# Kernel tuning notes

Hardware: AMD Instinct MI355X
Metric: run time of the kernel (lower is better)

## Reference

```python
import jax, jax.numpy as jnp
import numpy as np
from jax import lax

DN = ('NCHW', 'OIHW', 'NCHW')
EPS = 1e-12  # torch F.normalize eps


def _conv(x, w, b, groups=1):
    y = lax.conv_general_dilated(x, w, window_strides=(1, 1), padding='SAME',
                                 dimension_numbers=DN, feature_group_count=groups)
    return y + b[None, :, None, None]


def _l2norm(x):
    # normalize along last axis, matching torch.nn.functional.normalize
    n = jnp.sqrt(jnp.sum(x * x, axis=-1, keepdims=True))
    return x / jnp.maximum(n, EPS)


def setup_inputs() -> dict:
    key = jax.random.key(0)
    ks = jax.random.split(key, 5)
    dim, heads = 192, 8
    b, h, w = 4, 256, 256
    return {
        'x': jax.random.normal(ks[0], (b, dim, h, w), jnp.float32),
        'qkv_w': jax.random.normal(ks[1], (3 * dim, dim, 1, 1), jnp.float32) * 0.05,
        'qkv_b': jnp.zeros((3 * dim,), jnp.float32),
        'dw_w': jax.random.normal(ks[2], (3 * dim, 1, 3, 3), jnp.float32) * 0.05,
        'dw_b': jnp.zeros((3 * dim,), jnp.float32),
        'scale': jnp.ones((1, heads, 1, 1), jnp.float32),
        'proj_w': jax.random.normal(ks[3], (dim, dim, 1, 1), jnp.float32) * 0.05,
        'proj_b': jnp.zeros((dim,), jnp.float32),
    }


def reference(x, qkv_w, qkv_b, dw_w, dw_b, scale, proj_w, proj_b):
    b, c, h, w = x.shape
    heads = scale.shape[1]
    hc = c // heads  # per-head channels
    hw = h * w

    qkv = _conv(x, qkv_w, qkv_b)                       # [b, 3c, h, w]
    qkv = _conv(qkv, dw_w, dw_b, groups=3 * c)          # depthwise 3x3
    q, k, v = jnp.split(qkv, 3, axis=1)                 # each [b, c, h, w]

    # b (head c) h w -> b head c (h w)
    def heads_flat(t):
        return t.reshape(b, heads, hc, hw)

    q = _l2norm(heads_flat(q))
    k = _l2norm(heads_flat(k))
    v = heads_flat(v)

    attn = jnp.einsum('bncs,bnds->bncd', q, k) * scale   # [b, heads, hc, hc]
    attn = jax.nn.softmax(attn, axis=-1)
    out = jnp.einsum('bncd,bnds->bncs', attn, v)         # [b, heads, hc, hw]
    out = out.reshape(b, c, h, w)
    return _conv(out, proj_w, proj_b)
```

## Files before the change

### kernel.cpp

```cpp
#include <hip/hip_runtime.h>
#include <hip/hip_bf16.h>

typedef unsigned short u16;
typedef __attribute__((ext_vector_type(8))) short bf16x8;
typedef __attribute__((ext_vector_type(4))) float f32x4;

#define MFMA16(a,b,c) __builtin_amdgcn_mfma_f32_16x16x32_bf16(a,b,c,0,0,0)

__device__ __forceinline__ u16 f2bf(float f) {
  union { float f; unsigned u; } v; v.f = f;
  return (u16)((v.u + 0x7fffu + ((v.u >> 16) & 1u)) >> 16);
}
__device__ __forceinline__ float bf2f(u16 h) {
  union { unsigned u; float f; } v; v.u = ((unsigned)h) << 16;
  return v.f;
}
__device__ __forceinline__ int qkv_ch(int g, int c) {
  if (g < 8) return (c < 24) ? (g*24 + c) : (192 + g*24 + (c - 24));
  return 384 + (g - 8)*48 + c;
}

__global__ __launch_bounds__(256) void k0_wb(
    const float* __restrict__ qkv_w, const float* __restrict__ qkv_b,
    u16* __restrict__ Wb, float* __restrict__ Bp) {
  int j = blockIdx.x*256 + threadIdx.x;
  int m = j / 192, k = j % 192;
  Wb[j] = f2bf(qkv_w[qkv_ch(m/48, m%48)*192 + k]);
  if (j < 576) Bp[j] = qkv_b[qkv_ch(j/48, j%48)];
}

__global__ __launch_bounds__(512) void k1_qkv(
    const float* __restrict__ x, const u16* __restrict__ Wb,
    const float* __restrict__ Bp, u16* __restrict__ qkv1) {
  int blk = blockIdx.x;
  int bb = blk >> 9, nb = blk & 511;
  int s0 = nb << 7;
  int t = threadIdx.x;
  int lane = t & 63, wid = t >> 6;
  int lg = lane >> 4, lr = lane & 15;
  int wr = wid >> 1, wc = wid & 1;

  __shared__ __align__(16) u16 Bt[24*128*8];

  const float* xb = x + (size_t)bb*(192*65536) + s0;
  {
    int px4 = t & 31, kO = t >> 5;
    #pragma unroll
    for (int rnd = 0; rnd < 2; ++rnd, kO += 16) {
      if (kO < 24) {
        float4 f[8];
        #pragma unroll
        for (int j = 0; j < 8; ++j)
          f[j] = *(const float4*)(xb + (size_t)(kO*8 + j)*65536 + px4*4);
        #pragma unroll
        for (int e = 0; e < 4; ++e) {
          int px = px4*4 + e;
          bf16x8 hh;
          #pragma unroll
          for (int j = 0; j < 8; ++j)
            hh[j] = (short)f2bf(((const float*)&f[j])[e]);
          int byte = (kO*2048 + px*16) ^ ((px4 & 7) << 4);
          *(bf16x8*)((char*)Bt + byte) = hh;
        }
      }
    }
  }
  __syncthreads();

  #pragma unroll 1
  for (int pass = 0; pass < 3; ++pass) {
    int g = pass*4 + wr;
    bf16x8 af[3][6];
    #pragma unroll
    for (int mt = 0; mt < 3; ++mt) {
      const u16* wrp = Wb + (size_t)(g*48 + mt*16 + lr)*192 + lg*8;
      #pragma unroll
      for (int ks = 0; ks < 6; ++ks)
        af[mt][ks] = *(const bf16x8*)(wrp + ks*32);
    }
    f32x4 acc[3][4];
    #pragma unroll
    for (int mt = 0; mt < 3; ++mt)
      #pragma unroll
      for (int nt = 0; nt < 4; ++nt)
        acc[mt][nt] = (f32x4){0.f, 0.f, 0.f, 0.f};

    #pragma unroll
    for (int ks = 0; ks < 6; ++ks) {
      bf16x8 bf[4];
      #pragma unroll
      for (int nt = 0; nt < 4; ++nt) {
        int px = wc*64 + nt*16 + lr;
        int byte = ((ks*4 + lg)*2048 + px*16) ^ (((px >> 2) & 7) << 4);
        bf[nt] = *(const bf16x8*)((const char*)Bt + byte);
      }
      #pragma unroll
      for (int mt = 0; mt < 3; ++mt)
        #pragma unroll
        for (int nt = 0; nt < 4; ++nt)
          acc[mt][nt] = MFMA16(af[mt][ks], bf[nt], acc[mt][nt]);
    }

    u16* dst = qkv1 + ((size_t)(bb*12 + g)*65536 + s0)*48;
    #pragma unroll
    for (int mt = 0; mt < 3; ++mt) {
      float4 bv = *(const float4*)(Bp + g*48 + mt*16 + lg*4);
      #pragma unroll
      for (int nt = 0; nt < 4; ++nt) {
        int px = wc*64 + nt*16 + lr;
        ushort4 o;
        o.x = f2bf(acc[mt][nt][0] + bv.x);
        o.y = f2bf(acc[mt][nt][1] + bv.y);
        o.z = f2bf(acc[mt][nt][2] + bv.z);
        o.w = f2bf(acc[mt][nt][3] + bv.w);
        *(ushort4*)(dst + (size_t)px*48 + mt*16 + lg*4) = o;
      }
    }
  }
}

__global__ __launch_bounds__(256) void k2_dw(
    const u16* __restrict__ qkv1, const float* __restrict__ dw_w,
    const float* __restrict__ dw_b, u16* __restrict__ vd,
    float* __restrict__ partials) {
  int tile = blockIdx.x;
  int tx = tile & 15, ty = tile >> 4;
  int g  = blockIdx.y;
  int bb = blockIdx.z;
  int x0 = tx << 4, y0 = ty << 4;
  int t = threadIdx.x;

  __shared__ __align__(16) u16 buf0[9472];
  __shared__ __align__(16) u16 buf1[14784];
  __shared__ float w9[432];
  __shared__ float wb[48];
  float* stg = (float*)buf0;

  for (int j = t; j < 480; j += 256) {
    if (j < 432) { int c = j / 9; w9[j] = dw_w[qkv_ch(g, c)*9 + (j % 9)]; }
    else         { int c = j - 432; wb[c] = dw_b[qkv_ch(g, c)]; }
  }
  if (g < 8)
    for (int j = t; j < 2112; j += 256) buf1[12672 + j] = 0;

  const u16* src = qkv1 + (size_t)(bb*12 + g) * (65536*48);

  #pragma unroll 1
  for (int h = 0; h < 3; ++h) {
    if (h) __syncthreads();
    #pragma unroll
    for (int r = 0; r < 3; ++r) {
      int j = t + (r << 8);
      if (j < 648) {
        int hp = j >> 1, c16 = j & 1;
        int hr = hp / 18, hc = hp - hr*18;
        int hy = y0 - 1 + hr, hx = x0 - 1 + hc;
        uint4 v = {0u, 0u, 0u, 0u};
        if (hy >= 0 && hy < 256 && hx >= 0 && hx < 256)
          v = *(const uint4*)(src + ((size_t)hy*256 + hx)*48 + h*16 + c16*8);
        const u16* us = (const u16*)&v;
        int base = c16*(8*456 + 8) + hr*24 + hc;
        #pragma unroll
        for (int cc = 0; cc < 8; ++cc)
          buf0[base + cc*456] = us[cc];
      }
    }
    __syncthreads();

    {
      int lc = t & 15, row = t >> 4;
      int c = h*16 + lc;
      float wv[9];
      #pragma unroll
      for (int i = 0; i < 9; ++i) wv[i] = w9[c*9 + i];
      float bias = wb[c];
      int ibase = lc*456 + ((lc >> 3) << 3);
      float rowf[3][18];
      #pragma unroll
      for (int dy = 0; dy < 3; ++dy) {
        int base = ibase + (row + dy)*24;
        u16 hrow[18];
        *(uint4*)(hrow)      = *(const uint4*)(buf0 + base);
        *(uint4*)(hrow + 8)  = *(const uint4*)(buf0 + base + 8);
        *(uint*)(hrow + 16)  = *(const uint*)(buf0 + base + 16);
        #pragma unroll
        for (int i2 = 0; i2 < 18; ++i2) rowf[dy][i2] = bf2f(hrow[i2]);
      }
      float o[16];
      #pragma unroll
      for (int p = 0; p < 16; ++p) {
        float a = bias;
        #pragma unroll
        for (int dy = 0; dy < 3; ++dy)
          a += rowf[dy][p]*wv[dy*3] + rowf[dy][p+1]*wv[dy*3+1] + rowf[dy][p+2]*wv[dy*3+2];
        o[p] = a;
      }
      if (g < 8) {
        unsigned ow[8];
        #pragma unroll
        for (int i = 0; i < 8; ++i)
          asm volatile("v_cvt_pk_bf16_f32 %0, %1, %2"
                       : "=v"(ow[i]) : "v"(o[2*i]), "v"(o[2*i + 1]));
        u16* dsth = buf1 + c*264 + row*16;
        *(uint4*)(dsth)     = make_uint4(ow[0], ow[1], ow[2], ow[3]);
        *(uint4*)(dsth + 8) = make_uint4(ow[4], ow[5], ow[6], ow[7]);
      } else {
        int obase = row*792 + c;
        #pragma unroll
        for (int p = 0; p < 16; ++p)
          buf1[obase + p*48] = f2bf(o[p]);
      }
    }
  }
  __syncthreads();

  if (g < 8) {
    int lane = t & 63, w = t >> 6;
    int lr = lane & 15, lg = lane >> 4;
    f32x4 cc4[8];
    #pragma unroll
    for (int i = 0; i < 8; ++i) cc4[i] = (f32x4){0.f, 0.f, 0.f, 0.f};
    #pragma unroll
    for (int ks = 0; ks < 2; ++ks) {
      int pxb = w*64 + ks*32 + lg*8;
      bf16x8 aq[2], ak[2];
      aq[0] = *(const bf16x8*)(buf1 + (size_t)lr*264 + pxb);
      aq[1] = *(const bf16x8*)(buf1 + (size_t)(16 + lr)*264 + pxb);
      ak[0] = *(const bf16x8*)(buf1 + (size_t)(24 + lr)*264 + pxb);
      ak[1] = *(const bf16x8*)(buf1 + (size_t)(40 + lr)*264 + pxb);
      cc4[0] = MFMA16(aq[0], ak[0], cc4[0]);
      cc4[1] = MFMA16(aq[0], ak[1], cc4[1]);
      cc4[2] = MFMA16(aq[1], ak[0], cc4[2]);
      cc4[3] = MFMA16(aq[1], ak[1], cc4[3]);
      cc4[4] = MFMA16(aq[0], aq[0], cc4[4]);
      cc4[5] = MFMA16(aq[1], aq[1], cc4[5]);
      cc4[6] = MFMA16(ak[0], ak[0], cc4[6]);
      cc4[7] = MFMA16(ak[1], ak[1], cc4[7]);
    }
    #pragma unroll
    for (int tile2 = 0; tile2 < 4; ++tile2) {
      float* sp = stg + w*1088 + tile2*272 + lr;
      #pragma unroll
      for (int r = 0; r < 4; ++r)
        sp[(lg*4 + r)*17] = cc4[tile2][r];
    }
    {
      int r = lr - lg*4;
      if (r >= 0 && r < 4) {
        stg[4352 + w*96 + lr]      = cc4[4][r];
        stg[4352 + w*96 + 48 + lr] = cc4[6][r];
        if (lr < 8) {
          stg[4352 + w*96 + 16 + lr]      = cc4[5][r];
          stg[4352 + w*96 + 48 + 16 + lr] = cc4[7][r];
        }
      }
    }
    __syncthreads();
    float* pdst = partials + (((size_t)bb*256 + tile)*8 + g) * 640;
    for (int e = t; e < 624; e += 256) {
      float s = 0.f;
      if (e < 576) {
        int c = e / 24, d = e % 24;
        int off = ((c >> 4)*2 + (d >> 4))*272 + (c & 15)*17 + (d & 15);
        #pragma unroll
        for (int w2 = 0; w2 < 4; ++w2) s += stg[w2*1088 + off];
      } else {
        int cc2 = e - 576;
        int qk = cc2 / 24, ch = cc2 % 24;
        #pragma unroll
        for (int w2 = 0; w2 < 4; ++w2) s += stg[4352 + w2*96 + qk*48 + ch];
      }
      pdst[e] = s;
    }
  } else {
    u16* dst = vd + (size_t)bb * (65536*192);
    #pragma unroll
    for (int i = 0; i < 6; ++i) {
      int j = t + (i << 8);
      int pp = j / 6, c16 = j % 6;
      int py = pp >> 4, px = pp & 15;
      size_t s = (size_t)(y0 + py)*256 + (x0 + px);
      uint4 v = *(const uint4*)(buf1 + pp*48 + py*24 + c16*8);
      *(uint4*)(dst + s*192 + (g - 8)*48 + c16*8) = v;
    }
  }
}

__global__ __launch_bounds__(256) void k3a(
    const float* __restrict__ partials, float* __restrict__ G2) {
  int bb = blockIdx.x, h = blockIdx.y, ch = blockIdx.z;
  int t = threadIdx.x;
  for (int e = t; e < 624; e += 256) {
    const float* p = partials + ((size_t)(bb*256 + ch*32)*8 + h)*640 + e;
    float s = 0.f;
    #pragma unroll 4
    for (int blk = 0; blk < 32; ++blk) s += p[(size_t)blk * (8*640)];
    G2[(size_t)((bb*8 + h)*8 + ch)*640 + e] = s;
  }
}

__global__ __launch_bounds__(256) void k3b(
    const float* __restrict__ G2, const float* __restrict__ scale,
    const float* __restrict__ proj_w, u16* __restrict__ M) {
  int bb = blockIdx.x, h = blockIdx.y;
  int t = threadIdx.x;
  __shared__ float Gh[640];
  __shared__ float attn[24*24];
  for (int j = t; j < 640; j += 256) {
    float s = 0.f;
    #pragma unroll
    for (int ch = 0; ch < 8; ++ch)
      s += G2[(size_t)((bb*8 + h)*8 + ch)*640 + j];
    Gh[j] = s;
  }
  __syncthreads();
  if (t < 24) {
    int c = t;
    float qn = fmaxf(sqrtf(fmaxf(Gh[576 + c], 0.f)), 1e-12f);
    float sc = scale[h];
    float L[24];
    float mx = -1e30f;
    #pragma unroll
    for (int d = 0; d < 24; ++d) {
      float kn = fmaxf(sqrtf(fmaxf(Gh[600 + d], 0.f)), 1e-12f);
      L[d] = Gh[c*24 + d] / (qn * kn) * sc;
      mx = fmaxf(mx, L[d]);
    }
    float ssum = 0.f;
    #pragma unroll
    for (int d = 0; d < 24; ++d) { L[d] = __expf(L[d] - mx); ssum += L[d]; }
    float inv = 1.f / ssum;
    #pragma unroll
    for (int d = 0; d < 24; ++d) attn[c*24 + d] = L[d] * inv;
  }
  __syncthreads();
  for (int j = t; j < 4608; j += 256) {
    int co = j / 24, d = j % 24;
    const float* Pr = proj_w + co*192 + h*24;
    float s = 0.f;
    #pragma unroll
    for (int c = 0; c < 24; ++c) s += Pr[c] * attn[c*24 + d];
    M[(size_t)bb*36864 + co*192 + h*24 + d] = f2bf(s);
  }
}

__global__ __launch_bounds__(256) void k4_out(
    const u16* __restrict__ vd, const u16* __restrict__ M,
    const float* __restrict__ proj_b, float* __restrict__ out) {
  int p = blockIdx.x;
  int xcd = p & 7, q = p >> 3;
  int pr = xcd*512 + q;
  int bb = pr >> 10, nb = pr & 1023;
  int s0 = nb << 6;
  int t = threadIdx.x;
  int lane = t & 63, wid = t >> 6;
  int lg = lane >> 4, lr = lane & 15;

  const u16* Mb = M + (size_t)bb*36864;
  const u16* Bs = vd + ((size_t)bb*65536 + s0)*192;

  f32x4 acc[3][4];
  #pragma unroll
  for (int mt = 0; mt < 3; ++mt)
    #pragma unroll
    for (int nt = 0; nt < 4; ++nt)
      acc[mt][nt] = (f32x4){0.f, 0.f, 0.f, 0.f};

  #pragma unroll
  for (int ks = 0; ks < 6; ++ks) {
    bf16x8 bf[4], af[3];
    #pragma unroll
    for (int nt = 0; nt < 4; ++nt)
      bf[nt] = *(const bf16x8*)(Bs + (size_t)(nt*16 + lr)*192 + ks*32 + lg*8);
    #pragma unroll
    for (int mt = 0; mt < 3; ++mt)
      af[mt] = *(const bf16x8*)(Mb + (size_t)(wid*48 + mt*16 + lr)*192 + ks*32 + lg*8);
    #pragma unroll
    for (int mt = 0; mt < 3; ++mt)
      #pragma unroll
      for (int nt = 0; nt < 4; ++nt)
        acc[mt][nt] = MFMA16(af[mt], bf[nt], acc[mt][nt]);
  }

  float* dst = out + (size_t)bb*(192*65536) + s0;
  #pragma unroll
  for (int mt = 0; mt < 3; ++mt) {
    int m0 = wid*48 + mt*16 + lg*4;
    #pragma unroll
    for (int r = 0; r < 4; ++r) {
      float bias = proj_b[m0 + r];
      #pragma unroll
      for (int nt = 0; nt < 4; ++nt)
        dst[(size_t)(m0 + r)*65536 + nt*16 + lr] = acc[mt][nt][r] + bias;
    }
  }
}

extern "C" void kernel_launch(void* const* d_in, const int* in_sizes, int n_in,
                              void* d_out, int out_size, void* d_ws, size_t ws_size,
                              hipStream_t stream) {
  (void)in_sizes; (void)n_in; (void)out_size; (void)ws_size;
  const float* x      = (const float*)d_in[0];
  const float* qkv_w  = (const float*)d_in[1];
  const float* qkv_b  = (const float*)d_in[2];
  const float* dw_w   = (const float*)d_in[3];
  const float* dw_b   = (const float*)d_in[4];
  const float* scale  = (const float*)d_in[5];
  const float* proj_w = (const float*)d_in[6];
  const float* proj_b = (const float*)d_in[7];
  float* out = (float*)d_out;
  char* ws = (char*)d_ws;

  u16*   qkv1     = (u16*)(ws);
  u16*   vd       = (u16*)(ws + 301989888ULL);
  float* partials = (float*)(ws + 402653184ULL);
  u16*   Wb       = (u16*)(ws + 402653184ULL);
  float* Bp       = (float*)(ws + 402653184ULL + 221184ULL);
  float* G2       = (float*)(ws);
  u16*   M        = (u16*)(ws + 1048576ULL);

  k0_wb<<<dim3(432), dim3(256), 0, stream>>>(qkv_w, qkv_b, Wb, Bp);
  k1_qkv<<<dim3(2048), dim3(512), 0, stream>>>(x, Wb, Bp, qkv1);
  k2_dw<<<dim3(256, 12, 4), dim3(256), 0, stream>>>(qkv1, dw_w, dw_b, vd, partials);
  k3a<<<dim3(4, 8, 8), dim3(256), 0, stream>>>(partials, G2);
  k3b<<<dim3(4, 8), dim3(256), 0, stream>>>(G2, scale, proj_w, M);
  k4_out<<<dim3(4096), dim3(256), 0, stream>>>(vd, M, proj_b, out);
}
```

Baseline: 525.0 us.

## Shrink QKV GEMM tiles to 64 pixels, stream weights per k-step, use packed bf16 convert

The QKV 1x1-conv GEMM kernel now processes 64 pixels per block with 256 threads instead of 128 pixels with 512 threads, halving shared memory per block and requesting 5 blocks per CU. Weight fragments are now loaded per k-step instead of being held for all six k-steps, which lowers register pressure and should raise occupancy. Float-to-bf16 conversion now uses the hardware v_cvt_pk_bf16_f32 instruction in place of manual integer rounding. The trade-off is more global weight reads, since each block reloads the weights for twice as many tiles, and possible differences in rounding behaviour from the hardware convert.

New measurement: 566.7 us. +8.0%, slower.

```diff
diff --git a/kernel.cpp b/kernel.cpp
--- a/kernel.cpp
+++ b/kernel.cpp
@@ -29,22 +29,21 @@
   if (j < 576) Bp[j] = qkv_b[qkv_ch(j/48, j%48)];
 }
 
-__global__ __launch_bounds__(512) void k1_qkv(
+__global__ __launch_bounds__(256, 5) void k1_qkv(
     const float* __restrict__ x, const u16* __restrict__ Wb,
     const float* __restrict__ Bp, u16* __restrict__ qkv1) {
   int blk = blockIdx.x;
-  int bb = blk >> 9, nb = blk & 511;
-  int s0 = nb << 7;
+  int bb = blk >> 10, nb = blk & 1023;
+  int s0 = nb << 6;
   int t = threadIdx.x;
   int lane = t & 63, wid = t >> 6;
   int lg = lane >> 4, lr = lane & 15;
-  int wr = wid >> 1, wc = wid & 1;
-
-  __shared__ __align__(16) u16 Bt[24*128*8];
+
+  __shared__ __align__(16) u16 Bt[24*64*8];
 
   const float* xb = x + (size_t)bb*(192*65536) + s0;
   {
-    int px4 = t & 31, kO = t >> 5;
+    int px4 = t & 15, kO = t >> 4;
     #pragma unroll
     for (int rnd = 0; rnd < 2; ++rnd, kO += 16) {
       if (kO < 24) {
@@ -55,12 +54,17 @@
         #pragma unroll
         for (int e = 0; e < 4; ++e) {
           int px = px4*4 + e;
-          bf16x8 hh;
-          #pragma unroll
-          for (int j = 0; j < 8; ++j)
-            hh[j] = (short)f2bf(((const float*)&f[j])[e]);
-          int byte = (kO*2048 + px*16) ^ ((px4 & 7) << 4);
-          *(bf16x8*)((char*)Bt + byte) = hh;
+          unsigned w0, w1, w2, w3;
+          asm volatile("v_cvt_pk_bf16_f32 %0, %1, %2" : "=v"(w0)
+                       : "v"(((const float*)&f[0])[e]), "v"(((const float*)&f[1])[e]));
+          asm volatile("v_cvt_pk_bf16_f32 %0, %1, %2" : "=v"(w1)
+                       : "v"(((const float*)&f[2])[e]), "v"(((const float*)&f[3])[e]));
+          asm volatile("v_cvt_pk_bf16_f32 %0, %1, %2" : "=v"(w2)
+                       : "v"(((const float*)&f[4])[e]), "v"(((const float*)&f[5])[e]));
+          asm volatile("v_cvt_pk_bf16_f32 %0, %1, %2" : "=v"(w3)
+                       : "v"(((const float*)&f[6])[e]), "v"(((const float*)&f[7])[e]));
+          int byte = (kO*1024 + px*16) ^ ((px4 & 7) << 4);
+          *(uint4*)((char*)Bt + byte) = make_uint4(w0, w1, w2, w3);
         }
       }
     }
@@ -69,15 +73,7 @@
 
   #pragma unroll 1
   for (int pass = 0; pass < 3; ++pass) {
-    int g = pass*4 + wr;
-    bf16x8 af[3][6];
-    #pragma unroll
-    for (int mt = 0; mt < 3; ++mt) {
-      const u16* wrp = Wb + (size_t)(g*48 + mt*16 + lr)*192 + lg*8;
-      #pragma unroll
-      for (int ks = 0; ks < 6; ++ks)
-        af[mt][ks] = *(const bf16x8*)(wrp + ks*32);
-    }
+    int g = pass*4 + wid;
     f32x4 acc[3][4];
     #pragma unroll
     for (int mt = 0; mt < 3; ++mt)
@@ -87,18 +83,21 @@
 
     #pragma unroll
     for (int ks = 0; ks < 6; ++ks) {
-      bf16x8 bf[4];
+      bf16x8 af[3], bf[4];
+      #pragma unroll
+      for (int mt = 0; mt < 3; ++mt)
+        af[mt] = *(const bf16x8*)(Wb + (size_t)(g*48 + mt*16 + lr)*192 + ks*32 + lg*8);
       #pragma unroll
       for (int nt = 0; nt < 4; ++nt) {
-        int px = wc*64 + nt*16 + lr;
-        int byte = ((ks*4 + lg)*2048 + px*16) ^ (((px >> 2) & 7) << 4);
+        int px = nt*16 + lr;
+        int byte = ((ks*4 + lg)*1024 + px*16) ^ (((px >> 2) & 7) << 4);
         bf[nt] = *(const bf16x8*)((const char*)Bt + byte);
       }
       #pragma unroll
       for (int mt = 0; mt < 3; ++mt)
         #pragma unroll
         for (int nt = 0; nt < 4; ++nt)
-          acc[mt][nt] = MFMA16(af[mt][ks], bf[nt], acc[mt][nt]);
+          acc[mt][nt] = MFMA16(af[mt], bf[nt], acc[mt][nt]);
     }
 
     u16* dst = qkv1 + ((size_t)(bb*12 + g)*65536 + s0)*48;
@@ -107,13 +106,15 @@
       float4 bv = *(const float4*)(Bp + g*48 + mt*16 + lg*4);
       #pragma unroll
       for (int nt = 0; nt < 4; ++nt) {
-        int px = wc*64 + nt*16 + lr;
-        ushort4 o;
-        o.x = f2bf(acc[mt][nt][0] + bv.x);
-        o.y = f2bf(acc[mt][nt][1] + bv.y);
-        o.z = f2bf(acc[mt][nt][2] + bv.z);
-        o.w = f2bf(acc[mt][nt][3] + bv.w);
-        *(ushort4*)(dst + (size_t)px*48 + mt*16 + lg*4) = o;
+        int px = nt*16 + lr;
+        float a0 = acc[mt][nt][0] + bv.x;
+        float a1 = acc[mt][nt][1] + bv.y;
+        float a2 = acc[mt][nt][2] + bv.z;
+        float a3 = acc[mt][nt][3] + bv.w;
+        unsigned w0, w1;
+        asm volatile("v_cvt_pk_bf16_f32 %0, %1, %2" : "=v"(w0) : "v"(a0), "v"(a1));
+        asm volatile("v_cvt_pk_bf16_f32 %0, %1, %2" : "=v"(w1) : "v"(a2), "v"(a3));
+        *(uint2*)(dst + (size_t)px*48 + mt*16 + lg*4) = make_uint2(w0, w1);
       }
     }
   }
@@ -420,7 +421,7 @@
   u16*   M        = (u16*)(ws + 1048576ULL);
 
   k0_wb<<<dim3(432), dim3(256), 0, stream>>>(qkv_w, qkv_b, Wb, Bp);
-  k1_qkv<<<dim3(2048), dim3(512), 0, stream>>>(x, Wb, Bp, qkv1);
+  k1_qkv<<<dim3(4096), dim3(256), 0, stream>>>(x, Wb, Bp, qkv1);
   k2_dw<<<dim3(256, 12, 4), dim3(256), 0, stream>>>(qkv1, dw_w, dw_b, vd, partials);
   k3a<<<dim3(4, 8, 8), dim3(256), 0, stream>>>(partials, G2);
   k3b<<<dim3(4, 8), dim3(256), 0, stream>>>(G2, scale, proj_w, M);
```
